# Optimization experiments

Measured on AMD Instinct MI355X. Metric: run time of the kernel, lower is better.

Reference implementation:

```python
import jax, jax.numpy as jnp
import numpy as np

N = 100000
E = 1600000
F = 64
H = 64
C = 10


def setup_inputs() -> dict:
    key = jax.random.key(0)
    ks = jax.random.split(key, 8)
    x = jax.random.normal(ks[0], (N, F), dtype=jnp.float32)
    edge_index = jax.random.randint(ks[1], (2, E), 0, N, dtype=jnp.int64)
    s = 1.0 / np.sqrt(H)
    enc_w = jax.random.uniform(ks[2], (F, H), jnp.float32, -s, s)
    enc_b = jax.random.uniform(ks[3], (H,), jnp.float32, -s, s)
    proc_w = jax.random.uniform(ks[4], (H, H), jnp.float32, -s, s)
    proc_b = jax.random.uniform(ks[5], (H,), jnp.float32, -s, s)
    dec_w = jax.random.uniform(ks[6], (H, C), jnp.float32, -s, s)
    dec_b = jax.random.uniform(ks[7], (C,), jnp.float32, -s, s)
    return {"x": x, "edge_index": edge_index, "diameter": 6,
            "enc_w": enc_w, "enc_b": enc_b,
            "proc_w": proc_w, "proc_b": proc_b,
            "dec_w": dec_w, "dec_b": dec_b}


def reference(x, edge_index, diameter, enc_w, enc_b, proc_w, proc_b, dec_w, dec_b):
    # encoder
    h = x @ enc_w + enc_b  # [N, H]
    src = edge_index[0]
    dst = edge_index[1]
    n = x.shape[0]
    # GINConv (eps=0, aggr='max'): h = nn(h + scatter_max_j h_j)
    for _ in range(diameter):
        agg = jax.ops.segment_max(h[src], dst, num_segments=n)  # [N, H]
        agg = jnp.where(jnp.isfinite(agg), agg, 0.0)  # empty segments -> 0
        h = (h + agg) @ proc_w + proc_b
    # single decoder head, node-level log-softmax
    return jax.nn.log_softmax(h @ dec_w + dec_b, axis=-1)
```

## Files before the change

kernel.cpp:

```cpp
#include <hip/hip_runtime.h>
#include <hip/hip_fp16.h>
#include <math.h>


#define NPW 8
#define NPG 16
#define CAP 64

typedef unsigned short ushort_t;
typedef unsigned int uint_t;
typedef _Float16 half8 __attribute__((ext_vector_type(8)));
typedef float floatx4 __attribute__((ext_vector_type(4)));
typedef uint_t uintx4 __attribute__((ext_vector_type(4)));

__device__ __forceinline__ uint_t pkmax(uint_t a, uint_t b) {
    uint_t r;
    asm volatile("v_pk_max_f16 %0, %1, %2" : "=v"(r) : "v"(a), "v"(b));
    return r;
}
__device__ __forceinline__ uintx4 pkmax4(uintx4 a, uintx4 b) {
    uintx4 r;
    r.x = pkmax(a.x, b.x);
    r.y = pkmax(a.y, b.y);
    r.z = pkmax(a.z, b.z);
    r.w = pkmax(a.w, b.w);
    return r;
}
__device__ __forceinline__ uintx4 shmax4(uintx4 m, int msk) {
    uintx4 t;
    t.x = (uint_t)__shfl_xor((int)m.x, msk);
    t.y = (uint_t)__shfl_xor((int)m.y, msk);
    t.z = (uint_t)__shfl_xor((int)m.z, msk);
    t.w = (uint_t)__shfl_xor((int)m.w, msk);
    return pkmax4(m, t);
}
__device__ __forceinline__ ushort_t f2h(float x) {
    return __half_as_ushort(__float2half_rn(x));
}
__device__ __forceinline__ float h2f_lo(uint_t u) {
    return __half2float(__ushort_as_half((ushort_t)(u & 0xFFFF)));
}
__device__ __forceinline__ float h2f_hi(uint_t u) {
    return __half2float(__ushort_as_half((ushort_t)(u >> 16)));
}
__device__ __forceinline__ int uclamp(int i, int n) {
    uint_t u = (uint_t)i, un = (uint_t)n;
    return (int)(u < un ? u : un);
}

__global__ void prep_k(int* __restrict__ cur, int n,
                       ushort_t* __restrict__ ha, ushort_t* __restrict__ hb) {
    int i = blockIdx.x * blockDim.x + threadIdx.x;
    if (i < n) cur[i] = 0;
    if (blockIdx.x == 0 && threadIdx.x < 64) {
        ha[(size_t)n * 64 + threadIdx.x] = 0xFC00;
        hb[(size_t)n * 64 + threadIdx.x] = 0xFC00;
    }
}

__global__ __launch_bounds__(256) void scatter_xcd(const int* __restrict__ src,
                                                   const int* __restrict__ dst,
                                                   int E, int n,
                                                   int* __restrict__ cursor,
                                                   int* __restrict__ csr_src) {
    int part = blockIdx.x & 7;
    int bip = blockIdx.x >> 3;
    int nGroups = gridDim.x >> 3;
    int lo = (int)(((long long)part * n) >> 3);
    int hi = (int)(((long long)(part + 1) * n) >> 3);
    int stride = nGroups * blockDim.x;
    for (int i = bip * blockDim.x + threadIdx.x; i < E; i += stride) {
        int d = __builtin_nontemporal_load(&dst[i]);
        if (d >= lo && d < hi) {
            int s = __builtin_nontemporal_load(&src[i]);
            int pos = atomicAdd(&cursor[d], 1);
            if (pos < CAP) csr_src[(size_t)d * CAP + pos] = s;
        }
    }
}

__device__ __forceinline__ void gemm8(const float* __restrict__ Ws,
                                      const float (*hsw)[64],
                                      float bias, int lane, float acc[NPW]) {
#pragma unroll
    for (int r = 0; r < NPW; r++) acc[r] = bias;
#pragma unroll 1
    for (int kc = 0; kc < 8; kc++) {
        float wreg[8];
#pragma unroll
        for (int j = 0; j < 8; j++) wreg[j] = Ws[(kc * 8 + j) * 64 + lane];
#pragma unroll
        for (int r = 0; r < NPW; r++) {
            float4 a = *(const float4*)&hsw[r][kc * 8];
            float4 c = *(const float4*)&hsw[r][kc * 8 + 4];
            acc[r] = fmaf(a.x, wreg[0], acc[r]);
            acc[r] = fmaf(a.y, wreg[1], acc[r]);
            acc[r] = fmaf(a.z, wreg[2], acc[r]);
            acc[r] = fmaf(a.w, wreg[3], acc[r]);
            acc[r] = fmaf(c.x, wreg[4], acc[r]);
            acc[r] = fmaf(c.y, wreg[5], acc[r]);
            acc[r] = fmaf(c.z, wreg[6], acc[r]);
            acc[r] = fmaf(c.w, wreg[7], acc[r]);
        }
    }
}

__global__ __launch_bounds__(256, 4) void encode_k(const float* __restrict__ x,
                                                   const float* __restrict__ w,
                                                   const float* __restrict__ b,
                                                   ushort_t* __restrict__ h2, int n) {
    __shared__ float Ws[64 * 64];
    __shared__ float hs[4][NPW][64];
    {
        const float4* w4 = (const float4*)w;
        float4* s4 = (float4*)Ws;
        for (int i = threadIdx.x; i < 1024; i += 256) s4[i] = w4[i];
    }
    int wv = threadIdx.x >> 6;
    int lane = threadIdx.x & 63;
    int base = (blockIdx.x * 4 + wv) * NPW;

#pragma unroll
    for (int r = 0; r < NPW; r++) {
        int node = base + r;
        if (node < n) hs[wv][r][lane] = x[(size_t)node * 64 + lane];
    }
    __syncthreads();

    float bias = b[lane];
    float acc[NPW];
    gemm8(Ws, hs[wv], bias, lane, acc);

#pragma unroll
    for (int r = 0; r < NPW; r++) {
        int node = base + r;
        if (node < n) h2[(size_t)node * 64 + lane] = f2h(acc[r]);
    }
}

__device__ __forceinline__ void gin_body(const ushort_t* __restrict__ h2in,
                                         const int* __restrict__ degcur,
                                         const int* __restrict__ csr_src,
                                         const ushort_t* __restrict__ Wt,
                                         const float* __restrict__ bias,
                                         ushort_t* __restrict__ myhs,
                                         int base, int lane, int n) {
    int f8 = lane & 7;
    int sub3 = lane >> 3;
    const uintx4* hq = (const uintx4*)h2in;

#pragma unroll 2
    for (int rp = 0; rp < NPG; rp++) {
        int node = base + rp;
        bool v = node < n;
        int d = v ? degcur[node] : 0;
        d = (d > CAP) ? CAP : d;
        const int4* ip = (const int4*)&csr_src[(size_t)(v ? node : 0) * CAP];
        int4 i0 = ip[sub3];
        uintx4 a0 = hq[(size_t)uclamp(i0.x, n) * 8 + f8];
        uintx4 a1 = hq[(size_t)uclamp(i0.y, n) * 8 + f8];
        uintx4 a2 = hq[(size_t)uclamp(i0.z, n) * 8 + f8];
        uintx4 a3 = hq[(size_t)uclamp(i0.w, n) * 8 + f8];
        uintx4 m = pkmax4(pkmax4(a0, a1), pkmax4(a2, a3));
        if (d > 32) {
            int4 i1 = ip[8 + sub3];
            uintx4 c0 = hq[(size_t)uclamp(i1.x, n) * 8 + f8];
            uintx4 c1 = hq[(size_t)uclamp(i1.y, n) * 8 + f8];
            uintx4 c2 = hq[(size_t)uclamp(i1.z, n) * 8 + f8];
            uintx4 c3 = hq[(size_t)uclamp(i1.w, n) * 8 + f8];
            m = pkmax4(m, pkmax4(pkmax4(c0, c1), pkmax4(c2, c3)));
        }
        m = shmax4(m, 8);
        m = shmax4(m, 16);
        m = shmax4(m, 32);
        if (sub3 == 0 && v) {
            uintx4 s = hq[(size_t)node * 8 + f8];
            float r0 = h2f_lo(s.x), r1 = h2f_hi(s.x);
            float r2 = h2f_lo(s.y), r3 = h2f_hi(s.y);
            float r4 = h2f_lo(s.z), r5 = h2f_hi(s.z);
            float r6 = h2f_lo(s.w), r7 = h2f_hi(s.w);
            if (d > 0) {
                r0 += h2f_lo(m.x); r1 += h2f_hi(m.x);
                r2 += h2f_lo(m.y); r3 += h2f_hi(m.y);
                r4 += h2f_lo(m.z); r5 += h2f_hi(m.z);
                r6 += h2f_lo(m.w); r7 += h2f_hi(m.w);
            }
            uintx4 o;
            o.x = (uint_t)f2h(r0) | ((uint_t)f2h(r1) << 16);
            o.y = (uint_t)f2h(r2) | ((uint_t)f2h(r3) << 16);
            o.z = (uint_t)f2h(r4) | ((uint_t)f2h(r5) << 16);
            o.w = (uint_t)f2h(r6) | ((uint_t)f2h(r7) << 16);
            *(uintx4*)&myhs[rp * 72 + f8 * 8] = o;
        }
    }

    int m = lane & 15, quad = lane >> 4;
    float b0 = bias[m], b1 = bias[16 + m], b2 = bias[32 + m], b3 = bias[48 + m];
    floatx4 c0 = {0.f, 0.f, 0.f, 0.f}, c1 = c0, c2 = c0, c3 = c0;
#pragma unroll
    for (int kt = 0; kt < 2; kt++) {
        half8 a = *(const half8*)&myhs[m * 72 + kt * 32 + quad * 8];
        half8 w0 = *(const half8*)&Wt[(m) * 72 + kt * 32 + quad * 8];
        half8 w1 = *(const half8*)&Wt[(16 + m) * 72 + kt * 32 + quad * 8];
        half8 w2 = *(const half8*)&Wt[(32 + m) * 72 + kt * 32 + quad * 8];
        half8 w3 = *(const half8*)&Wt[(48 + m) * 72 + kt * 32 + quad * 8];
        c0 = __builtin_amdgcn_mfma_f32_16x16x32_f16(a, w0, c0, 0, 0, 0);
        c1 = __builtin_amdgcn_mfma_f32_16x16x32_f16(a, w1, c1, 0, 0, 0);
        c2 = __builtin_amdgcn_mfma_f32_16x16x32_f16(a, w2, c2, 0, 0, 0);
        c3 = __builtin_amdgcn_mfma_f32_16x16x32_f16(a, w3, c3, 0, 0, 0);
    }
#pragma unroll
    for (int i = 0; i < 4; i++) {
        int row = quad * 4 + i;
        myhs[row * 72 + m]      = f2h(c0[i] + b0);
        myhs[row * 72 + 16 + m] = f2h(c1[i] + b1);
        myhs[row * 72 + 32 + m] = f2h(c2[i] + b2);
        myhs[row * 72 + 48 + m] = f2h(c3[i] + b3);
    }
}

__global__ __launch_bounds__(256, 6) void gin16_k(const ushort_t* __restrict__ h2in,
                                                  ushort_t* __restrict__ h2out,
                                                  const int* __restrict__ degcur,
                                                  const int* __restrict__ csr_src,
                                                  const float* __restrict__ w,
                                                  const float* __restrict__ bias,
                                                  int n) {
    __shared__ __align__(16) ushort_t Wt[64 * 72];
    __shared__ __align__(16) ushort_t hs2[4][NPG * 72];

    for (int i = threadIdx.x; i < 4096; i += 256) {
        int k = i >> 6, nn = i & 63;
        Wt[nn * 72 + k] = f2h(w[i]);
    }
    __syncthreads();

    int wv = threadIdx.x >> 6, lane = threadIdx.x & 63;
    int base = (blockIdx.x * 4 + wv) * NPG;
    ushort_t* myhs = hs2[wv];

    gin_body(h2in, degcur, csr_src, Wt, bias, myhs, base, lane, n);

#pragma unroll
    for (int r = 0; r < NPG; r++) {
        int node = base + r;
        if (node < n) h2out[(size_t)node * 64 + lane] = myhs[r * 72 + lane];
    }
}

__global__ __launch_bounds__(256, 6) void gin16d_k(const ushort_t* __restrict__ h2in,
                                                   const int* __restrict__ degcur,
                                                   const int* __restrict__ csr_src,
                                                   const float* __restrict__ w,
                                                   const float* __restrict__ bias,
                                                   const float* __restrict__ dw,
                                                   const float* __restrict__ db,
                                                   float* __restrict__ out,
                                                   int n) {
    __shared__ __align__(16) ushort_t Wt[64 * 72];
    __shared__ __align__(16) ushort_t hs2[4][NPG * 72];
    __shared__ __align__(16) float dws[64 * 16];

    for (int i = threadIdx.x; i < 4096; i += 256) {
        int k = i >> 6, nn = i & 63;
        Wt[nn * 72 + k] = f2h(w[i]);
    }
    for (int i = threadIdx.x; i < 1024; i += 256) {
        int k = i >> 4, c = i & 15;
        dws[i] = (c < 10) ? dw[k * 10 + c] : 0.0f;
    }
    __syncthreads();

    int wv = threadIdx.x >> 6, lane = threadIdx.x & 63;
    int base = (blockIdx.x * 4 + wv) * NPG;
    ushort_t* myhs = hs2[wv];

    gin_body(h2in, degcur, csr_src, Wt, bias, myhs, base, lane, n);

    int m = lane & 15, quad = lane >> 4;
    float l[10];
#pragma unroll
    for (int c = 0; c < 10; c++) l[c] = 0.0f;
#pragma unroll
    for (int kk = 0; kk < 16; kk++) {
        int k = quad * 16 + kk;
        float hv = __half2float(__ushort_as_half(myhs[m * 72 + k]));
        const float* wr = &dws[k * 16];
        float4 w0 = *(const float4*)wr;
        float4 w1 = *(const float4*)(wr + 4);
        float2 w2 = *(const float2*)(wr + 8);
        l[0] = fmaf(hv, w0.x, l[0]);
        l[1] = fmaf(hv, w0.y, l[1]);
        l[2] = fmaf(hv, w0.z, l[2]);
        l[3] = fmaf(hv, w0.w, l[3]);
        l[4] = fmaf(hv, w1.x, l[4]);
        l[5] = fmaf(hv, w1.y, l[5]);
        l[6] = fmaf(hv, w1.z, l[6]);
        l[7] = fmaf(hv, w1.w, l[7]);
        l[8] = fmaf(hv, w2.x, l[8]);
        l[9] = fmaf(hv, w2.y, l[9]);
    }
#pragma unroll
    for (int c = 0; c < 10; c++) {
        l[c] += __shfl_xor(l[c], 16);
        l[c] += __shfl_xor(l[c], 32);
    }
    if (quad == 0) {
        int node = base + m;
        if (node < n) {
            float mx = -INFINITY;
#pragma unroll
            for (int c = 0; c < 10; c++) { l[c] += db[c]; mx = fmaxf(mx, l[c]); }
            float sum = 0.0f;
#pragma unroll
            for (int c = 0; c < 10; c++) sum += expf(l[c] - mx);
            float lse = mx + logf(sum);
#pragma unroll
            for (int c = 0; c < 10; c++) out[(size_t)node * 10 + c] = l[c] - lse;
        }
    }
}

extern "C" void kernel_launch(void* const* d_in, const int* in_sizes, int n_in,
                              void* d_out, int out_size, void* d_ws, size_t ws_size,
                              hipStream_t stream) {
    const float* x     = (const float*)d_in[0];
    const int*   ei    = (const int*)d_in[1];
    const float* enc_w = (const float*)d_in[3];
    const float* enc_b = (const float*)d_in[4];
    const float* proc_w = (const float*)d_in[5];
    const float* proc_b = (const float*)d_in[6];
    const float* dec_w = (const float*)d_in[7];
    const float* dec_b = (const float*)d_in[8];
    float* out = (float*)d_out;

    const int n = in_sizes[0] / 64;
    const int E = in_sizes[1] / 2;
    const int* src = ei;
    const int* dst = ei + E;

    char* p = (char*)d_ws;
    ushort_t* h_a = (ushort_t*)p;    p += (size_t)(n + 1) * 64 * sizeof(ushort_t);
    ushort_t* h_b = (ushort_t*)p;    p += (size_t)(n + 1) * 64 * sizeof(ushort_t);
    int* cur = (int*)p;              p += (size_t)n * sizeof(int);
    int* csr = (int*)p;              p += (size_t)n * CAP * sizeof(int);

    const int gN = (n + 255) / 256;
    const int gTileE = (n + 4 * NPW - 1) / (4 * NPW);
    const int gTileG = (n + 4 * NPG - 1) / (4 * NPG);

    prep_k<<<gN, 256, 0, stream>>>(cur, n, h_a, h_b);
    scatter_xcd<<<2048, 256, 0, stream>>>(src, dst, E, n, cur, csr);

    encode_k<<<gTileE, 256, 0, stream>>>(x, enc_w, enc_b, h_a, n);

    ushort_t* hi = h_a;
    ushort_t* ho = h_b;
    for (int it = 0; it < 5; it++) {
        gin16_k<<<gTileG, 256, 0, stream>>>(hi, ho, cur, csr, proc_w, proc_b, n);
        ushort_t* t = hi; hi = ho; ho = t;
    }

    gin16d_k<<<gTileG, 256, 0, stream>>>(hi, cur, csr, proc_w, proc_b,
                                         dec_w, dec_b, out, n);
}
```

Before: 427.1 us.

## Fuse edge scatter and node encoder into one heterogeneous kernel launch

Merges the CSR-building scatter kernel and the encoder GEMM into a single launch. The first SCB blocks do the edge scatter and the remaining blocks do the encoding, so the two independent stages can run concurrently and one launch is saved. The encoder also drops its shared-memory staging and syncthreads. It now broadcasts x values with wavefront shuffles and reads weights straight from global/L1. The risks are more shuffle instructions per FMA and higher register pressure. The heterogeneous blocks may also balance poorly across CUs.

```diff
diff --git a/kernel.cpp b/kernel.cpp
--- a/kernel.cpp
+++ b/kernel.cpp
@@ -6,6 +6,7 @@
 #define NPW 8
 #define NPG 16
 #define CAP 64
+#define SCB 2048
 
 typedef unsigned short ushort_t;
 typedef unsigned int uint_t;
@@ -58,83 +59,60 @@
     }
 }
 
-__global__ __launch_bounds__(256) void scatter_xcd(const int* __restrict__ src,
-                                                   const int* __restrict__ dst,
-                                                   int E, int n,
-                                                   int* __restrict__ cursor,
-                                                   int* __restrict__ csr_src) {
-    int part = blockIdx.x & 7;
-    int bip = blockIdx.x >> 3;
-    int nGroups = gridDim.x >> 3;
-    int lo = (int)(((long long)part * n) >> 3);
-    int hi = (int)(((long long)(part + 1) * n) >> 3);
-    int stride = nGroups * blockDim.x;
-    for (int i = bip * blockDim.x + threadIdx.x; i < E; i += stride) {
-        int d = __builtin_nontemporal_load(&dst[i]);
-        if (d >= lo && d < hi) {
-            int s = __builtin_nontemporal_load(&src[i]);
-            int pos = atomicAdd(&cursor[d], 1);
-            if (pos < CAP) csr_src[(size_t)d * CAP + pos] = s;
-        }
-    }
-}
-
-__device__ __forceinline__ void gemm8(const float* __restrict__ Ws,
-                                      const float (*hsw)[64],
-                                      float bias, int lane, float acc[NPW]) {
-#pragma unroll
-    for (int r = 0; r < NPW; r++) acc[r] = bias;
+__global__ __launch_bounds__(256) void scatter_encode_k(
+        const int* __restrict__ src, const int* __restrict__ dst,
+        int E, int n,
+        int* __restrict__ cursor, int* __restrict__ csr_src,
+        const float* __restrict__ x, const float* __restrict__ w,
+        const float* __restrict__ b, ushort_t* __restrict__ h2) {
+    if (blockIdx.x < SCB) {
+        int part = blockIdx.x & 7;
+        int bip = blockIdx.x >> 3;
+        int nGroups = SCB >> 3;
+        int lo = (int)(((long long)part * n) >> 3);
+        int hi = (int)(((long long)(part + 1) * n) >> 3);
+        int stride = nGroups * blockDim.x;
+        for (int i = bip * blockDim.x + threadIdx.x; i < E; i += stride) {
+            int d = __builtin_nontemporal_load(&dst[i]);
+            if (d >= lo && d < hi) {
+                int s = __builtin_nontemporal_load(&src[i]);
+                int pos = atomicAdd(&cursor[d], 1);
+                if (pos < CAP) csr_src[(size_t)d * CAP + pos] = s;
+            }
+        }
+    } else {
+        int wv = threadIdx.x >> 6;
+        int lane = threadIdx.x & 63;
+        int base = ((blockIdx.x - SCB) * 4 + wv) * NPW;
+
+        float xr[NPW];
+#pragma unroll
+        for (int r = 0; r < NPW; r++) {
+            int node = base + r;
+            xr[r] = (node < n) ? x[(size_t)node * 64 + lane] : 0.0f;
+        }
+        float bias = b[lane];
+        float acc[NPW];
+#pragma unroll
+        for (int r = 0; r < NPW; r++) acc[r] = bias;
 #pragma unroll 1
-    for (int kc = 0; kc < 8; kc++) {
-        float wreg[8];
-#pragma unroll
-        for (int j = 0; j < 8; j++) wreg[j] = Ws[(kc * 8 + j) * 64 + lane];
+        for (int kc = 0; kc < 8; kc++) {
+            float wreg[8];
+#pragma unroll
+            for (int j = 0; j < 8; j++) wreg[j] = w[(kc * 8 + j) * 64 + lane];
+#pragma unroll
+            for (int r = 0; r < NPW; r++) {
+#pragma unroll
+                for (int j = 0; j < 8; j++) {
+                    acc[r] = fmaf(__shfl(xr[r], kc * 8 + j), wreg[j], acc[r]);
+                }
+            }
+        }
 #pragma unroll
         for (int r = 0; r < NPW; r++) {
-            float4 a = *(const float4*)&hsw[r][kc * 8];
-            float4 c = *(const float4*)&hsw[r][kc * 8 + 4];
-            acc[r] = fmaf(a.x, wreg[0], acc[r]);
-            acc[r] = fmaf(a.y, wreg[1], acc[r]);
-            acc[r] = fmaf(a.z, wreg[2], acc[r]);
-            acc[r] = fmaf(a.w, wreg[3], acc[r]);
-            acc[r] = fmaf(c.x, wreg[4], acc[r]);
-            acc[r] = fmaf(c.y, wreg[5], acc[r]);
-            acc[r] = fmaf(c.z, wreg[6], acc[r]);
-            acc[r] = fmaf(c.w, wreg[7], acc[r]);
-        }
-    }
-}
-
-__global__ __launch_bounds__(256, 4) void encode_k(const float* __restrict__ x,
-                                                   const float* __restrict__ w,
-                                                   const float* __restrict__ b,
-                                                   ushort_t* __restrict__ h2, int n) {
-    __shared__ float Ws[64 * 64];
-    __shared__ float hs[4][NPW][64];
-    {
-        const float4* w4 = (const float4*)w;
-        float4* s4 = (float4*)Ws;
-        for (int i = threadIdx.x; i < 1024; i += 256) s4[i] = w4[i];
-    }
-    int wv = threadIdx.x >> 6;
-    int lane = threadIdx.x & 63;
-    int base = (blockIdx.x * 4 + wv) * NPW;
-
-#pragma unroll
-    for (int r = 0; r < NPW; r++) {
-        int node = base + r;
-        if (node < n) hs[wv][r][lane] = x[(size_t)node * 64 + lane];
-    }
-    __syncthreads();
-
-    float bias = b[lane];
-    float acc[NPW];
-    gemm8(Ws, hs[wv], bias, lane, acc);
-
-#pragma unroll
-    for (int r = 0; r < NPW; r++) {
-        int node = base + r;
-        if (node < n) h2[(size_t)node * 64 + lane] = f2h(acc[r]);
+            int node = base + r;
+            if (node < n) h2[(size_t)node * 64 + lane] = f2h(acc[r]);
+        }
     }
 }
 
@@ -350,9 +328,8 @@
     const int gTileG = (n + 4 * NPG - 1) / (4 * NPG);
 
     prep_k<<<gN, 256, 0, stream>>>(cur, n, h_a, h_b);
-    scatter_xcd<<<2048, 256, 0, stream>>>(src, dst, E, n, cur, csr);
-
-    encode_k<<<gTileE, 256, 0, stream>>>(x, enc_w, enc_b, h_a, n);
+    scatter_encode_k<<<SCB + gTileE, 256, 0, stream>>>(src, dst, E, n, cur, csr,
+                                                       x, enc_w, enc_b, h_a);
 
     ushort_t* hi = h_a;
     ushort_t* ho = h_b;
```

New measurement: 477.2 us. 11.7% more time.
